# Optimization experiments

Measured on AMD Instinct MI355X. Metric: run time of the kernel, lower is better.

Reference implementation:

```python
import math
import jax, jax.numpy as jnp
import numpy as np

ALPHA = 12.0  # agg_alpha
TAU = 0.07


def setup_inputs() -> dict:
    key = jax.random.key(0)
    kq, kk, kqm, kkm = jax.random.split(key, 4)
    B, Lq, O, Lk, D = 64, 32, 128, 256, 128
    q = jax.random.normal(kq, (B, Lq, D), dtype=jnp.float32)
    k = jax.random.normal(kk, (O, Lk, D), dtype=jnp.float32)
    # True = padding token (masked out)
    q_mask = jax.random.bernoulli(kqm, 0.1, (B, Lq))
    k_mask = jax.random.bernoulli(kkm, 0.1, (O, Lk))
    logit_scale = jnp.asarray(math.log(1.0 / TAU), dtype=jnp.float32)
    return {"q": q, "k": k, "q_mask": q_mask, "k_mask": k_mask,
            "logit_scale": logit_scale}


def _l2norm(x, eps=1e-12):
    # torch F.normalize: x / max(||x||_2, eps)
    n = jnp.sqrt(jnp.sum(x * x, axis=-1, keepdims=True))
    return x / jnp.maximum(n, eps)


def reference(q, k, q_mask, k_mask, logit_scale):
    B, Lq, D = q.shape
    O, Lk, _ = k.shape
    qn = _l2norm(q)
    kn = _l2norm(k)
    # S: [B, O, Lq, Lk] full similarity tensor (the kernel-headroom intermediate)
    S = jnp.einsum('bid,ojd->boij', qn, kn)
    m = q_mask[:, None, :, None] | k_mask[None, :, None, :]
    S = jnp.where(m, -jnp.inf, S)
    # softmax-pool over Lk: logsumexp(alpha*S)/alpha, then sum over Lq
    s = jax.nn.logsumexp(ALPHA * S, axis=-1) / ALPHA  # [B, O, Lq]
    s = jnp.sum(s, axis=-1)                            # [B, O]
    s = jnp.where(jnp.isfinite(s), s, jnp.zeros_like(s))
    # length_norm = 'sqrt'
    s = s / (math.sqrt(Lq * Lk) + 1e-06)
    # learnable temperature, exp clamped at 100
    scale = jnp.minimum(jnp.exp(logit_scale), 100.0)
    return s * scale
```

## Files before the change

kernel.cpp:

```cpp
#include <hip/hip_runtime.h>
#include <math.h>


#define ALPHA 12.0f

constexpr int B_  = 64;
constexpr int LQ  = 32;
constexpr int O_  = 128;
constexpr int LK  = 256;
constexpr int D_  = 128;
constexpr int LDH = D_ + 8;

typedef _Float16 half8 __attribute__((ext_vector_type(8)));
typedef _Float16 half4_t __attribute__((ext_vector_type(4)));
typedef float    f32x4 __attribute__((ext_vector_type(4)));

__global__ __launch_bounds__(256)
void prep_kernel(const int* __restrict__ q_mask,
                 float* __restrict__ out,
                 int* __restrict__ ws)
{
    __shared__ int anyb[B_];
    const int t = threadIdx.x;
    if (t < B_) anyb[t] = 0;
    __syncthreads();
    #pragma unroll
    for (int r = 0; r < 8; ++r) {
        int idx = t + 256 * r;
        if (q_mask[idx] != 0) atomicOr(&anyb[idx >> 5], 1);
    }
    __syncthreads();
    float4* o4 = (float4*)out;
    #pragma unroll
    for (int r = 0; r < 8; ++r)
        o4[t + 256 * r] = make_float4(0.f, 0.f, 0.f, 0.f);
    if (t < 64) {
        bool live = (anyb[t] == 0);
        unsigned long long m = __ballot(live);
        if (live) {
            int rank = __popcll(m & ((1ull << t) - 1ull));
            ws[1 + rank] = t;
        }
        if (t == 0) ws[0] = (int)__popcll(m);
    }
}

__global__ __launch_bounds__(256, 2)
void colbert_main_kernel(const float* __restrict__ q,
                         const float* __restrict__ k,
                         const int*  __restrict__ k_mask,
                         const float* __restrict__ logit_scale,
                         const int*  __restrict__ ws,
                         float* __restrict__ out)
{
    __shared__ _Float16 kl[LK][LDH];
    __shared__ _Float16 ql[LQ][LDH];
    __shared__ float rk[LK];
    __shared__ float bj[LK];
    __shared__ float rqa[LQ];
    __shared__ float part[2][LQ];

    const int t     = threadIdx.x;
    const int lane  = t & 63;
    const int w     = t >> 6;
    const int row16 = lane & 15;
    const int quad  = lane >> 4;

    const int M     = ws[0];
    const int ntask = M * O_;

    for (int task = blockIdx.x; task < ntask; task += gridDim.x) {
        __syncthreads();
        const int b = ws[1 + (task >> 7)];
        const int o = task & (O_ - 1);

        const float4* qg = (const float4*)(q + (size_t)b * LQ * D_);
        #pragma unroll
        for (int r = 0; r < 4; ++r) {
            int idx = t + 256 * r;
            float4 v = qg[idx];
            int i = idx >> 5, c4 = idx & 31;
            half4_t h;
            h[0] = (_Float16)v.x; h[1] = (_Float16)v.y;
            h[2] = (_Float16)v.z; h[3] = (_Float16)v.w;
            *(half4_t*)&ql[i][c4 * 4] = h;
        }
        const float4* kg = (const float4*)(k + (size_t)o * LK * D_);
        #pragma unroll
        for (int r = 0; r < 32; ++r) {
            int idx = t + 256 * r;
            float4 v = kg[idx];
            int j = idx >> 5, c4 = idx & 31;
            half4_t h;
            h[0] = (_Float16)v.x; h[1] = (_Float16)v.y;
            h[2] = (_Float16)v.z; h[3] = (_Float16)v.w;
            *(half4_t*)&kl[j][c4 * 4] = h;
        }
        __syncthreads();

        if (t < LQ) {
            float ss = 0.f;
            #pragma unroll
            for (int p = 0; p < 16; ++p) {
                half8 h = *(const half8*)&ql[t][p * 8];
                #pragma unroll
                for (int e = 0; e < 8; ++e) {
                    float x = (float)h[e];
                    ss = fmaf(x, x, ss);
                }
            }
            rqa[t] = ALPHA / fmaxf(sqrtf(ss), 1e-12f);
        }
        {
            float ss = 0.f;
            #pragma unroll
            for (int p = 0; p < 16; ++p) {
                half8 h = *(const half8*)&kl[t][p * 8];
                #pragma unroll
                for (int e = 0; e < 8; ++e) {
                    float x = (float)h[e];
                    ss = fmaf(x, x, ss);
                }
            }
            rk[t] = 1.0f / fmaxf(sqrtf(ss), 1e-12f);
            bj[t] = (k_mask[o * LK + t] != 0) ? -1e30f : 0.0f;
        }
        __syncthreads();

        const int i0 = (w >> 1) * 16;
        const int j0 = (w & 1) * 128;

        half8 afrag[4];
        #pragma unroll
        for (int kk = 0; kk < 4; ++kk)
            afrag[kk] = *(const half8*)&ql[i0 + row16][kk * 32 + quad * 8];

        float rqv[4];
        #pragma unroll
        for (int rg = 0; rg < 4; ++rg)
            rqv[rg] = rqa[i0 + quad * 4 + rg];

        float esum[4] = {0.f, 0.f, 0.f, 0.f};
        #pragma unroll
        for (int c = 0; c < 8; ++c) {
            const int jt = j0 + c * 16;
            f32x4 acc = {0.f, 0.f, 0.f, 0.f};
            #pragma unroll
            for (int kk = 0; kk < 4; ++kk) {
                half8 bfrag = *(const half8*)&kl[jt + row16][kk * 32 + quad * 8];
                acc = __builtin_amdgcn_mfma_f32_16x16x32_f16(afrag[kk], bfrag,
                                                             acc, 0, 0, 0);
            }
            const float rkj = rk[jt + row16];
            const float bb  = bj[jt + row16];
            #pragma unroll
            for (int rg = 0; rg < 4; ++rg)
                esum[rg] += __expf(acc[rg] * rqv[rg] * rkj + bb);
        }
        #pragma unroll
        for (int rg = 0; rg < 4; ++rg) {
            float e = esum[rg];
            e += __shfl_xor(e, 1);
            e += __shfl_xor(e, 2);
            e += __shfl_xor(e, 4);
            e += __shfl_xor(e, 8);
            esum[rg] = e;
        }
        if (row16 == 0) {
            #pragma unroll
            for (int rg = 0; rg < 4; ++rg)
                part[w & 1][i0 + quad * 4 + rg] = esum[rg];
        }
        __syncthreads();

        if (t < 64) {
            float s = 0.f, lse = 0.f;
            bool badrow = false;
            if (t < LQ) {
                s = part[0][t] + part[1][t];
                badrow = (s <= 0.f);
                lse = __logf(fmaxf(s, 1e-38f));
            }
            unsigned long long zb = __ballot(badrow);
            float tot = lse;
            tot += __shfl_xor(tot, 32);
            tot += __shfl_xor(tot, 16);
            tot += __shfl_xor(tot, 8);
            tot += __shfl_xor(tot, 4);
            tot += __shfl_xor(tot, 2);
            tot += __shfl_xor(tot, 1);
            if (t == 0) {
                float res = 0.f;
                if (zb == 0ULL) {
                    float scale  = fminf(__expf(logit_scale[0]), 100.0f);
                    float inv_ln = 1.0f / (sqrtf((float)(LQ * LK)) + 1e-6f);
                    res = (tot * (1.0f / ALPHA)) * inv_ln * scale;
                }
                out[b * O_ + o] = res;
            }
        }
    }
}

extern "C" void kernel_launch(void* const* d_in, const int* in_sizes, int n_in,
                              void* d_out, int out_size, void* d_ws, size_t ws_size,
                              hipStream_t stream) {
    const float* q           = (const float*)d_in[0];
    const float* k           = (const float*)d_in[1];
    const int*   q_mask      = (const int*)d_in[2];
    const int*   k_mask      = (const int*)d_in[3];
    const float* logit_scale = (const float*)d_in[4];
    float* out = (float*)d_out;
    int*   ws  = (int*)d_ws;

    prep_kernel<<<1, 256, 0, stream>>>(q_mask, out, ws);
    colbert_main_kernel<<<512, 256, 0, stream>>>(q, k, k_mask, logit_scale,
                                                 ws, out);
}
```

Measured before the change: 78.73 us.

## Fuse mask-prep into main kernel and reuse K tile across live batches

Removes the separate prep kernel: each block now computes the live-batch list from q_mask itself and zeroes the outputs for dead batches. The grid changes to one block per key object. Each block converts and normalizes its K tile once, then loops over all live query batches, instead of reloading K for every (b,o) task. This removes one kernel launch and the redundant K loads and norm computations. In exchange, the grid is smaller (128 blocks) and the live batches are processed serially within each block, which lowers parallelism.

```diff
diff --git a/kernel.cpp b/kernel.cpp
--- a/kernel.cpp
+++ b/kernel.cpp
@@ -11,47 +11,17 @@
 constexpr int D_  = 128;
 constexpr int LDH = D_ + 8;
 
-typedef _Float16 half8 __attribute__((ext_vector_type(8)));
+typedef _Float16 half8   __attribute__((ext_vector_type(8)));
 typedef _Float16 half4_t __attribute__((ext_vector_type(4)));
-typedef float    f32x4 __attribute__((ext_vector_type(4)));
-
-__global__ __launch_bounds__(256)
-void prep_kernel(const int* __restrict__ q_mask,
-                 float* __restrict__ out,
-                 int* __restrict__ ws)
-{
-    __shared__ int anyb[B_];
-    const int t = threadIdx.x;
-    if (t < B_) anyb[t] = 0;
-    __syncthreads();
-    #pragma unroll
-    for (int r = 0; r < 8; ++r) {
-        int idx = t + 256 * r;
-        if (q_mask[idx] != 0) atomicOr(&anyb[idx >> 5], 1);
-    }
-    __syncthreads();
-    float4* o4 = (float4*)out;
-    #pragma unroll
-    for (int r = 0; r < 8; ++r)
-        o4[t + 256 * r] = make_float4(0.f, 0.f, 0.f, 0.f);
-    if (t < 64) {
-        bool live = (anyb[t] == 0);
-        unsigned long long m = __ballot(live);
-        if (live) {
-            int rank = __popcll(m & ((1ull << t) - 1ull));
-            ws[1 + rank] = t;
-        }
-        if (t == 0) ws[0] = (int)__popcll(m);
-    }
-}
-
-__global__ __launch_bounds__(256, 2)
-void colbert_main_kernel(const float* __restrict__ q,
-                         const float* __restrict__ k,
-                         const int*  __restrict__ k_mask,
-                         const float* __restrict__ logit_scale,
-                         const int*  __restrict__ ws,
-                         float* __restrict__ out)
+typedef float    f32x4   __attribute__((ext_vector_type(4)));
+
+__global__ __launch_bounds__(256, 1)
+void colbert_fused_kernel(const float* __restrict__ q,
+                          const float* __restrict__ k,
+                          const int*  __restrict__ q_mask,
+                          const int*  __restrict__ k_mask,
+                          const float* __restrict__ logit_scale,
+                          float* __restrict__ out)
 {
     __shared__ _Float16 kl[LK][LDH];
     __shared__ _Float16 ql[LQ][LDH];
@@ -59,20 +29,76 @@
     __shared__ float bj[LK];
     __shared__ float rqa[LQ];
     __shared__ float part[2][LQ];
-
+    __shared__ int   deadf[B_];
+    __shared__ int   lbm[B_ + 1];
+
+    const int o     = blockIdx.x;
     const int t     = threadIdx.x;
     const int lane  = t & 63;
     const int w     = t >> 6;
     const int row16 = lane & 15;
     const int quad  = lane >> 4;
 
-    const int M     = ws[0];
-    const int ntask = M * O_;
-
-    for (int task = blockIdx.x; task < ntask; task += gridDim.x) {
-        __syncthreads();
-        const int b = ws[1 + (task >> 7)];
-        const int o = task & (O_ - 1);
+    {
+        const int4* qm4 = (const int4*)q_mask;
+        int4 a0 = qm4[t * 2], a1 = qm4[t * 2 + 1];
+        int any = a0.x | a0.y | a0.z | a0.w | a1.x | a1.y | a1.z | a1.w;
+        any |= __shfl_xor(any, 1);
+        any |= __shfl_xor(any, 2);
+        if ((t & 3) == 0) {
+            int b = t >> 2;
+            deadf[b] = any;
+            if (any) out[b * O_ + o] = 0.0f;
+        }
+    }
+    __syncthreads();
+    if (t < 64) {
+        bool live = (deadf[t] == 0);
+        unsigned long long m = __ballot(live);
+        if (live) {
+            int rank = __popcll(m & ((1ull << t) - 1ull));
+            lbm[1 + rank] = t;
+        }
+        if (t == 0) lbm[0] = (int)__popcll(m);
+    }
+    __syncthreads();
+    const int M = lbm[0];
+    if (M == 0) return;
+
+    {
+        const float4* kg = (const float4*)(k + (size_t)o * LK * D_);
+        #pragma unroll 8
+        for (int r = 0; r < 32; ++r) {
+            int idx = t + 256 * r;
+            float4 v = kg[idx];
+            int j = idx >> 5, c4 = idx & 31;
+            half4_t h;
+            h[0] = (_Float16)v.x; h[1] = (_Float16)v.y;
+            h[2] = (_Float16)v.z; h[3] = (_Float16)v.w;
+            *(half4_t*)&kl[j][c4 * 4] = h;
+        }
+    }
+    __syncthreads();
+    {
+        float ss = 0.f;
+        #pragma unroll
+        for (int p = 0; p < 16; ++p) {
+            half8 h = *(const half8*)&kl[t][p * 8];
+            #pragma unroll
+            for (int e = 0; e < 8; ++e) {
+                float x = (float)h[e];
+                ss = fmaf(x, x, ss);
+            }
+        }
+        rk[t] = 1.0f / fmaxf(sqrtf(ss), 1e-12f);
+        bj[t] = (k_mask[o * LK + t] != 0) ? -1e30f : 0.0f;
+    }
+
+    const float scale  = fminf(__expf(logit_scale[0]), 100.0f);
+    const float inv_ln = 1.0f / (sqrtf((float)(LQ * LK)) + 1e-6f);
+
+    for (int m = 0; m < M; ++m) {
+        const int b = lbm[1 + m];
 
         const float4* qg = (const float4*)(q + (size_t)b * LQ * D_);
         #pragma unroll
@@ -85,17 +111,6 @@
             h[2] = (_Float16)v.z; h[3] = (_Float16)v.w;
             *(half4_t*)&ql[i][c4 * 4] = h;
         }
-        const float4* kg = (const float4*)(k + (size_t)o * LK * D_);
-        #pragma unroll
-        for (int r = 0; r < 32; ++r) {
-            int idx = t + 256 * r;
-            float4 v = kg[idx];
-            int j = idx >> 5, c4 = idx & 31;
-            half4_t h;
-            h[0] = (_Float16)v.x; h[1] = (_Float16)v.y;
-            h[2] = (_Float16)v.z; h[3] = (_Float16)v.w;
-            *(half4_t*)&kl[j][c4 * 4] = h;
-        }
         __syncthreads();
 
         if (t < LQ) {
@@ -110,20 +125,6 @@
                 }
             }
             rqa[t] = ALPHA / fmaxf(sqrtf(ss), 1e-12f);
-        }
-        {
-            float ss = 0.f;
-            #pragma unroll
-            for (int p = 0; p < 16; ++p) {
-                half8 h = *(const half8*)&kl[t][p * 8];
-                #pragma unroll
-                for (int e = 0; e < 8; ++e) {
-                    float x = (float)h[e];
-                    ss = fmaf(x, x, ss);
-                }
-            }
-            rk[t] = 1.0f / fmaxf(sqrtf(ss), 1e-12f);
-            bj[t] = (k_mask[o * LK + t] != 0) ? -1e30f : 0.0f;
         }
         __syncthreads();
 
@@ -191,11 +192,8 @@
             tot += __shfl_xor(tot, 1);
             if (t == 0) {
                 float res = 0.f;
-                if (zb == 0ULL) {
-                    float scale  = fminf(__expf(logit_scale[0]), 100.0f);
-                    float inv_ln = 1.0f / (sqrtf((float)(LQ * LK)) + 1e-6f);
+                if (zb == 0ULL)
                     res = (tot * (1.0f / ALPHA)) * inv_ln * scale;
-                }
                 out[b * O_ + o] = res;
             }
         }
@@ -211,9 +209,7 @@
     const int*   k_mask      = (const int*)d_in[3];
     const float* logit_scale = (const float*)d_in[4];
     float* out = (float*)d_out;
-    int*   ws  = (int*)d_ws;
-
-    prep_kernel<<<1, 256, 0, stream>>>(q_mask, out, ws);
-    colbert_main_kernel<<<512, 256, 0, stream>>>(q, k, k_mask, logit_scale,
-                                                 ws, out);
+
+    colbert_fused_kernel<<<O_, 256, 0, stream>>>(q, k, q_mask, k_mask,
+                                                 logit_scale, out);
 }
```

New measurement: 76.11 us. 3.3% less time.
